# Performance work log

Hardware: AMD Instinct MI355X
Metric: run time of the kernel (lower is better)

## Reference

```python
import jax, jax.numpy as jnp
import numpy as np

B, T, D = 4, 2048, 1024
H = 16
HD = D // H  # 64
SCALE = 1.0 / np.sqrt(HD).astype(np.float32)


def setup_inputs() -> dict:
    key = jax.random.key(0)
    ks = jax.random.split(key, 5)
    std = 0.02
    return {
        "x": jax.random.normal(ks[0], (B, T, D), dtype=jnp.float32),
        "wq": jax.random.normal(ks[1], (D, D), dtype=jnp.float32) * std,
        "wk": jax.random.normal(ks[2], (D, D), dtype=jnp.float32) * std,
        "wv": jax.random.normal(ks[3], (D, D), dtype=jnp.float32) * std,
        "wo": jax.random.normal(ks[4], (D, D), dtype=jnp.float32) * std,
    }


def _shape(t):
    # [B,T,D] -> [B,H,T,HD]
    Bt, Tt, _ = t.shape
    return t.reshape(Bt, Tt, H, HD).transpose(0, 2, 1, 3)


def reference(x, wq, wk, wv, wo):
    # Linear layers are y = x @ W^T (torch nn.Linear semantics, no bias)
    q = _shape(x @ wq.T)  # [B,H,T,HD]
    k = _shape(x @ wk.T)
    v = _shape(x @ wv.T)
    att = jnp.einsum("bhqd,bhkd->bhqk", q, k) * SCALE  # [B,H,T,T]
    # causal mask: -inf strictly above diagonal
    causal = jnp.triu(jnp.full((T, T), -jnp.inf, dtype=att.dtype), k=1)
    att = att + causal[None, None, :, :]
    att = jax.nn.softmax(att.astype(jnp.float32), axis=-1).astype(att.dtype)
    # dropout prob = 0.0 -> identity
    y = jnp.einsum("bhqk,bhkd->bhqd", att, v)  # [B,H,T,HD]
    y = y.transpose(0, 2, 1, 3).reshape(B, T, D)
    return y @ wo.T
```

## Files before the change

kernel.cpp:

```cpp
#include <hip/hip_runtime.h>
#include <hip/hip_bf16.h>

#define BB 4
#define TT 2048
#define DDIM 1024
#define HH 16
#define HD 64

typedef __bf16 bf16_t;
typedef __bf16 bf16x4 __attribute__((ext_vector_type(4)));
typedef __bf16 bf16x8 __attribute__((ext_vector_type(8)));
typedef float f32x4 __attribute__((ext_vector_type(4)));

#define GLOAD_LDS(gp, lp) \
    __builtin_amdgcn_global_load_lds( \
        (const __attribute__((address_space(1))) void*)(gp), \
        (__attribute__((address_space(3))) void*)(lp), 16, 0, 0)

__global__ __launch_bounds__(256) void cvt_f32_bf16(
    const float* __restrict__ src, bf16_t* __restrict__ dst, size_t n8)
{
    size_t i = (size_t)blockIdx.x * blockDim.x + threadIdx.x;
    const size_t stride = (size_t)gridDim.x * blockDim.x;
    for (; i < n8; i += stride) {
        const f32x4 a = ((const f32x4*)src)[2 * i];
        const f32x4 b = ((const f32x4*)src)[2 * i + 1];
        bf16x8 v;
#pragma unroll
        for (int j = 0; j < 4; j++) { v[j] = (bf16_t)a[j]; v[4 + j] = (bf16_t)b[j]; }
        ((bf16x8*)dst)[i] = v;
    }
}

__global__ __launch_bounds__(256) void cvt_wpack(
    const float* __restrict__ s0, const float* __restrict__ s1,
    const float* __restrict__ s2, const float* __restrict__ s3,
    bf16_t* __restrict__ dst)
{
    const size_t n8 = (size_t)4 * DDIM * DDIM / 8;
    size_t i = (size_t)blockIdx.x * blockDim.x + threadIdx.x;
    const size_t stride = (size_t)gridDim.x * blockDim.x;
    for (; i < n8; i += stride) {
        const int sel = (int)(i >> 17);
        const float* s = sel == 0 ? s0 : sel == 1 ? s1 : sel == 2 ? s2 : s3;
        const size_t off8 = i & ((1u << 17) - 1);
        const f32x4 a = ((const f32x4*)s)[2 * off8];
        const f32x4 b = ((const f32x4*)s)[2 * off8 + 1];
        bf16x8 v;
#pragma unroll
        for (int j = 0; j < 4; j++) { v[j] = (bf16_t)a[j]; v[4 + j] = (bf16_t)b[j]; }
        ((bf16x8*)dst)[i] = v;
    }
}

__global__ __launch_bounds__(256) void gemm_qkv(
    const bf16_t* __restrict__ A, const bf16_t* __restrict__ Wqkv,
    bf16_t* __restrict__ Qo, bf16_t* __restrict__ Ko, bf16_t* __restrict__ Vto,
    int M, int K)
{
    __shared__ alignas(16) bf16_t As[128 * 32];
    __shared__ alignas(16) bf16_t Bs[128 * 32];

    const int tid  = threadIdx.x;
    const int lane = tid & 63;
    const int w    = tid >> 6;
    const int quad = lane >> 4;
    const int l15  = lane & 15;
    const int wm   = (w >> 1) * 64;
    const int wn   = (w & 1) * 64;
    const int tileN = blockIdx.x * 128;
    const int tileM = blockIdx.y * 128;

    const f32x4 vzero = {0.f, 0.f, 0.f, 0.f};
    f32x4 acc[4][4];
#pragma unroll
    for (int i = 0; i < 4; i++)
#pragma unroll
        for (int j = 0; j < 4; j++) acc[i][j] = vzero;

    const int lrow = lane >> 2;
    const int lcol = (lane & 3) * 8;

    for (int k0 = 0; k0 < K; k0 += 32) {
        __syncthreads();
#pragma unroll
        for (int q = 0; q < 2; q++) {
            const int r0 = w * 32 + q * 16;
            GLOAD_LDS(&A[(size_t)(tileM + r0 + lrow) * K + k0 + lcol], &As[r0 * 32]);
            GLOAD_LDS(&Wqkv[(size_t)(tileN + r0 + lrow) * K + k0 + lcol], &Bs[r0 * 32]);
        }
        __syncthreads();

        bf16x8 af[4], bf[4];
#pragma unroll
        for (int i = 0; i < 4; i++)
            af[i] = *(bf16x8*)&As[(wm + i * 16 + l15) * 32 + quad * 8];
#pragma unroll
        for (int j = 0; j < 4; j++)
            bf[j] = *(bf16x8*)&Bs[(wn + j * 16 + l15) * 32 + quad * 8];
#pragma unroll
        for (int i = 0; i < 4; i++)
#pragma unroll
            for (int j = 0; j < 4; j++)
                acc[i][j] = __builtin_amdgcn_mfma_f32_16x16x32_bf16(
                    af[i], bf[j], acc[i][j], 0, 0, 0);
    }

    const int region = tileN >> 10;
#pragma unroll
    for (int i = 0; i < 4; i++) {
        const int row = tileM + wm + i * 16 + quad * 4;
#pragma unroll
        for (int j = 0; j < 4; j++) {
            const int ncol = tileN + wn + j * 16 + l15;
            if (region == 2) {
                const int cl = ncol - 2048;
                const int h = cl >> 6, d = cl & 63;
                const int bb = row >> 11, tloc = row & (TT - 1);
                bf16x4 pk;
#pragma unroll
                for (int r = 0; r < 4; r++) pk[r] = (bf16_t)acc[i][j][r];
                *(bf16x4*)&Vto[(((size_t)bb * HH + h) * HD + d) * TT + tloc] = pk;
            } else {
                bf16_t* dst = (region == 0) ? Qo : Ko;
                const int cl = ncol & 1023;
#pragma unroll
                for (int r = 0; r < 4; r++)
                    dst[(size_t)(row + r) * DDIM + cl] = (bf16_t)acc[i][j][r];
            }
        }
    }
}

__global__ __launch_bounds__(256) void gemm_out(
    const bf16_t* __restrict__ A, const bf16_t* __restrict__ Bm,
    float* __restrict__ C, int M, int N, int K)
{
    __shared__ alignas(16) bf16_t As[64 * 32];
    __shared__ alignas(16) bf16_t Bs[128 * 32];

    const int tid  = threadIdx.x;
    const int lane = tid & 63;
    const int w    = tid >> 6;
    const int quad = lane >> 4;
    const int l15  = lane & 15;
    const int wm   = (w >> 1) * 32;
    const int wn   = (w & 1) * 64;
    const int tileN = blockIdx.x * 128;
    const int tileM = blockIdx.y * 64;

    const f32x4 vzero = {0.f, 0.f, 0.f, 0.f};
    f32x4 acc[2][4];
#pragma unroll
    for (int i = 0; i < 2; i++)
#pragma unroll
        for (int j = 0; j < 4; j++) acc[i][j] = vzero;

    const int lrow = lane >> 2;
    const int lcol = (lane & 3) * 8;

    for (int k0 = 0; k0 < K; k0 += 32) {
        __syncthreads();
        GLOAD_LDS(&A[(size_t)(tileM + w * 16 + lrow) * K + k0 + lcol], &As[w * 16 * 32]);
#pragma unroll
        for (int q = 0; q < 2; q++) {
            const int r0 = w * 32 + q * 16;
            GLOAD_LDS(&Bm[(size_t)(tileN + r0 + lrow) * K + k0 + lcol], &Bs[r0 * 32]);
        }
        __syncthreads();

        bf16x8 af[2], bf[4];
#pragma unroll
        for (int i = 0; i < 2; i++)
            af[i] = *(bf16x8*)&As[(wm + i * 16 + l15) * 32 + quad * 8];
#pragma unroll
        for (int j = 0; j < 4; j++)
            bf[j] = *(bf16x8*)&Bs[(wn + j * 16 + l15) * 32 + quad * 8];
#pragma unroll
        for (int i = 0; i < 2; i++)
#pragma unroll
            for (int j = 0; j < 4; j++)
                acc[i][j] = __builtin_amdgcn_mfma_f32_16x16x32_bf16(
                    af[i], bf[j], acc[i][j], 0, 0, 0);
    }

#pragma unroll
    for (int i = 0; i < 2; i++) {
#pragma unroll
        for (int r = 0; r < 4; r++) {
            const int row = tileM + wm + i * 16 + quad * 4 + r;
#pragma unroll
            for (int j = 0; j < 4; j++)
                C[(size_t)row * N + tileN + wn + j * 16 + l15] = acc[i][j][r];
        }
    }
}

__global__ __launch_bounds__(256, 4) void attn_causal(
    const bf16_t* __restrict__ Q, const bf16_t* __restrict__ Kg,
    const bf16_t* __restrict__ Vt_g, bf16_t* __restrict__ Y)
{
    __shared__ alignas(16) bf16_t Ks[64 * 72];
    __shared__ alignas(16) bf16_t Vt[64 * 72];
    __shared__ alignas(16) bf16_t Ps[4][16 * 72];

    const int tid  = threadIdx.x;
    const int lane = tid & 63;
    const int w    = tid >> 6;
    const int quad = lane >> 4;
    const int l15  = lane & 15;
    const int bh   = blockIdx.x;
    const int qp   = blockIdx.y;
    const int b = bh >> 4, h = bh & 15;

    const int stg_row = tid >> 3;
    const int stg_c8  = (tid & 7) * 8;

    const f32x4 vzero = {0.f, 0.f, 0.f, 0.f};
    bf16x8 ones;
#pragma unroll
    for (int j = 0; j < 8; j++) ones[j] = (l15 == 0) ? (bf16_t)1.0f : (bf16_t)0.0f;

#pragma unroll 1
    for (int half = 0; half < 2; half++) {
        const int qtile = half ? (31 - qp) : qp;
        const int qbase = qtile * 64;

        bf16x8 qf[2];
        {
            const size_t rq = (size_t)(b * TT + qbase + w * 16 + l15) * DDIM + h * 64;
            qf[0] = *(const bf16x8*)&Q[rq + quad * 8];
            qf[1] = *(const bf16x8*)&Q[rq + 32 + quad * 8];
        }

        f32x4 o[4], o4;
#pragma unroll
        for (int c = 0; c < 4; c++) o[c] = vzero;
        o4 = vzero;

        for (int kt = 0; kt <= qtile; kt++) {
            const int kbase = kt * 64;
            __syncthreads();
#pragma unroll
            for (int p = 0; p < 2; p++) {
                const int r = stg_row + p * 32;
                *(bf16x8*)&Ks[r * 72 + stg_c8] =
                    *(const bf16x8*)&Kg[(size_t)(b * TT + kbase + r) * DDIM + h * 64 + stg_c8];
                *(bf16x8*)&Vt[r * 72 + stg_c8] =
                    *(const bf16x8*)&Vt_g[((size_t)bh * HD + r) * TT + kbase + stg_c8];
            }
            __syncthreads();

            f32x4 s[4];
#pragma unroll
            for (int c = 0; c < 4; c++) {
                s[c] = vzero;
#pragma unroll
                for (int ss = 0; ss < 2; ss++) {
                    bf16x8 kf = *(bf16x8*)&Ks[(c * 16 + l15) * 72 + ss * 32 + quad * 8];
                    s[c] = __builtin_amdgcn_mfma_f32_16x16x32_bf16(qf[ss], kf, s[c], 0, 0, 0);
                }
            }

            const bool diag = (kt == qtile);
#pragma unroll
            for (int r = 0; r < 4; r++) {
                const int rrow = w * 16 + quad * 4 + r;
#pragma unroll
                for (int c = 0; c < 4; c++) {
                    float sv = s[c][r] * 0.125f;
                    if (diag && (c * 16 + l15 > rrow)) sv = -1e30f;
                    const int pchunk = (c * 2 + (l15 >> 3)) ^ quad;
                    Ps[w][(quad * 4 + r) * 72 + (pchunk << 3) + (l15 & 7)] =
                        (bf16_t)__expf(sv);
                }
            }

#pragma unroll
            for (int ss = 0; ss < 2; ss++) {
                bf16x8 pf = *(bf16x8*)&Ps[w][l15 * 72 +
                                             (((ss * 4 + quad) ^ (l15 >> 2)) << 3)];
#pragma unroll
                for (int c = 0; c < 4; c++) {
                    bf16x8 vf = *(bf16x8*)&Vt[(c * 16 + l15) * 72 + ss * 32 + quad * 8];
                    o[c] = __builtin_amdgcn_mfma_f32_16x16x32_bf16(pf, vf, o[c], 0, 0, 0);
                }
                o4 = __builtin_amdgcn_mfma_f32_16x16x32_bf16(pf, ones, o4, 0, 0, 0);
            }
        }

#pragma unroll
        for (int r = 0; r < 4; r++) {
            const float lsum = __shfl(o4[r], lane & 48, 64);
            const float inv = 1.0f / lsum;
            const int q = qbase + w * 16 + quad * 4 + r;
#pragma unroll
            for (int c = 0; c < 4; c++)
                Y[(size_t)(b * TT + q) * DDIM + h * 64 + c * 16 + l15] =
                    (bf16_t)(o[c][r] * inv);
        }
    }
}

extern "C" void kernel_launch(void* const* d_in, const int* in_sizes, int n_in,
                              void* d_out, int out_size, void* d_ws, size_t ws_size,
                              hipStream_t stream) {
    (void)in_sizes; (void)n_in; (void)out_size;
    const float* x  = (const float*)d_in[0];
    float* out = (float*)d_out;

    const int M = BB * TT;
    const size_t REGION = (size_t)M * DDIM;
    const size_t WREG   = (size_t)DDIM * DDIM;
    const size_t BATCH  = (size_t)TT * DDIM;
    bf16_t* ws = (bf16_t*)d_ws;

    if (ws_size >= (72ull << 20)) {
        bf16_t* xb  = ws;
        bf16_t* wpk = ws + REGION;
        bf16_t* Qb  = wpk + 4 * WREG;
        bf16_t* Kb  = Qb + REGION;
        bf16_t* Vtb = Kb + REGION;

        cvt_f32_bf16<<<1024, 256, 0, stream>>>(x, xb, REGION / 8);
        cvt_wpack<<<512, 256, 0, stream>>>(
            (const float*)d_in[1], (const float*)d_in[2],
            (const float*)d_in[3], (const float*)d_in[4], wpk);

        gemm_qkv<<<dim3(24, M / 128), 256, 0, stream>>>(
            xb, wpk, Qb, Kb, Vtb, M, DDIM);
        attn_causal<<<dim3(BB * HH, 16), 256, 0, stream>>>(Qb, Kb, Vtb, Qb);
        gemm_out<<<dim3(8, M / 64), 256, 0, stream>>>(
            Qb, wpk + 3 * WREG, out, M, DDIM, DDIM);
    } else {
        bf16_t* wpk = ws;
        bf16_t* xbb = ws + 4 * WREG;
        bf16_t* Qb  = xbb + BATCH;
        bf16_t* Kb  = Qb + BATCH;
        bf16_t* Vtb = Kb + BATCH;

        cvt_wpack<<<512, 256, 0, stream>>>(
            (const float*)d_in[1], (const float*)d_in[2],
            (const float*)d_in[3], (const float*)d_in[4], wpk);

        for (int b = 0; b < BB; b++) {
            const float* x_b = x + (size_t)b * BATCH;
            float* out_b = out + (size_t)b * BATCH;
            cvt_f32_bf16<<<512, 256, 0, stream>>>(x_b, xbb, BATCH / 8);
            gemm_qkv<<<dim3(24, TT / 128), 256, 0, stream>>>(
                xbb, wpk, Qb, Kb, Vtb, TT, DDIM);
            attn_causal<<<dim3(HH, 16), 256, 0, stream>>>(Qb, Kb, Vtb, Qb);
            gemm_out<<<dim3(8, TT / 64), 256, 0, stream>>>(
                Qb, wpk + 3 * WREG, out_b, TT, DDIM, DDIM);
        }
    }
}
```

Before: 272.1 us.

## Double GEMM K-tile with swizzled LDS and widen attention query strips to 128

Both projection GEMMs now stage 64-wide K slices per barrier pair instead of 32, using an XOR-swizzled LDS layout to avoid bank conflicts, which halves the number of sync points per tile. The attention kernel has each wave handle 32 query rows (two MFMA row blocks), so every K/V tile loaded into LDS is reused across twice as many queries, and the grid is halved to 8 strips per head. The cost is more registers and LDS per block; the occupancy hint drops from 4 to 2 blocks, and there are fewer attention blocks in flight.

After: 266.9 us. No clear change (-1.9%).

```diff
diff --git a/kernel.cpp b/kernel.cpp
--- a/kernel.cpp
+++ b/kernel.cpp
@@ -53,13 +53,21 @@
     }
 }
 
+__device__ __forceinline__ void stage8(const bf16_t* __restrict__ g, int ld,
+                                       bf16_t* __restrict__ ldsbase, int lane)
+{
+    const int rr = lane >> 3;
+    const int cc = (lane & 7) ^ ((rr & 1) << 2);
+    GLOAD_LDS(&g[(size_t)rr * ld + cc * 8], ldsbase);
+}
+
 __global__ __launch_bounds__(256) void gemm_qkv(
     const bf16_t* __restrict__ A, const bf16_t* __restrict__ Wqkv,
     bf16_t* __restrict__ Qo, bf16_t* __restrict__ Ko, bf16_t* __restrict__ Vto,
     int M, int K)
 {
-    __shared__ alignas(16) bf16_t As[128 * 32];
-    __shared__ alignas(16) bf16_t Bs[128 * 32];
+    __shared__ alignas(16) bf16_t As[128 * 64];
+    __shared__ alignas(16) bf16_t Bs[128 * 64];
 
     const int tid  = threadIdx.x;
     const int lane = tid & 63;
@@ -78,32 +86,35 @@
 #pragma unroll
         for (int j = 0; j < 4; j++) acc[i][j] = vzero;
 
-    const int lrow = lane >> 2;
-    const int lcol = (lane & 3) * 8;
-
-    for (int k0 = 0; k0 < K; k0 += 32) {
+    const int par4 = (l15 & 1) << 2;
+
+    for (int k0 = 0; k0 < K; k0 += 64) {
         __syncthreads();
 #pragma unroll
-        for (int q = 0; q < 2; q++) {
-            const int r0 = w * 32 + q * 16;
-            GLOAD_LDS(&A[(size_t)(tileM + r0 + lrow) * K + k0 + lcol], &As[r0 * 32]);
-            GLOAD_LDS(&Wqkv[(size_t)(tileN + r0 + lrow) * K + k0 + lcol], &Bs[r0 * 32]);
+        for (int q = 0; q < 4; q++) {
+            const int r0 = w * 32 + q * 8;
+            stage8(&A[(size_t)(tileM + r0) * K + k0], K, &As[r0 * 64], lane);
+            stage8(&Wqkv[(size_t)(tileN + r0) * K + k0], K, &Bs[r0 * 64], lane);
         }
         __syncthreads();
 
-        bf16x8 af[4], bf[4];
-#pragma unroll
-        for (int i = 0; i < 4; i++)
-            af[i] = *(bf16x8*)&As[(wm + i * 16 + l15) * 32 + quad * 8];
-#pragma unroll
-        for (int j = 0; j < 4; j++)
-            bf[j] = *(bf16x8*)&Bs[(wn + j * 16 + l15) * 32 + quad * 8];
-#pragma unroll
-        for (int i = 0; i < 4; i++)
+#pragma unroll
+        for (int ss = 0; ss < 2; ss++) {
+            const int phys = ((ss * 4 + quad) ^ par4) << 3;
+            bf16x8 af[4], bf[4];
+#pragma unroll
+            for (int i = 0; i < 4; i++)
+                af[i] = *(bf16x8*)&As[(wm + i * 16 + l15) * 64 + phys];
 #pragma unroll
             for (int j = 0; j < 4; j++)
-                acc[i][j] = __builtin_amdgcn_mfma_f32_16x16x32_bf16(
-                    af[i], bf[j], acc[i][j], 0, 0, 0);
+                bf[j] = *(bf16x8*)&Bs[(wn + j * 16 + l15) * 64 + phys];
+#pragma unroll
+            for (int i = 0; i < 4; i++)
+#pragma unroll
+                for (int j = 0; j < 4; j++)
+                    acc[i][j] = __builtin_amdgcn_mfma_f32_16x16x32_bf16(
+                        af[i], bf[j], acc[i][j], 0, 0, 0);
+        }
     }
 
     const int region = tileN >> 10;
@@ -136,8 +147,8 @@
     const bf16_t* __restrict__ A, const bf16_t* __restrict__ Bm,
     float* __restrict__ C, int M, int N, int K)
 {
-    __shared__ alignas(16) bf16_t As[64 * 32];
-    __shared__ alignas(16) bf16_t Bs[128 * 32];
+    __shared__ alignas(16) bf16_t As[64 * 64];
+    __shared__ alignas(16) bf16_t Bs[128 * 64];
 
     const int tid  = threadIdx.x;
     const int lane = tid & 63;
@@ -156,32 +167,39 @@
 #pragma unroll
         for (int j = 0; j < 4; j++) acc[i][j] = vzero;
 
-    const int lrow = lane >> 2;
-    const int lcol = (lane & 3) * 8;
-
-    for (int k0 = 0; k0 < K; k0 += 32) {
+    const int par4 = (l15 & 1) << 2;
+
+    for (int k0 = 0; k0 < K; k0 += 64) {
         __syncthreads();
-        GLOAD_LDS(&A[(size_t)(tileM + w * 16 + lrow) * K + k0 + lcol], &As[w * 16 * 32]);
 #pragma unroll
         for (int q = 0; q < 2; q++) {
-            const int r0 = w * 32 + q * 16;
-            GLOAD_LDS(&Bm[(size_t)(tileN + r0 + lrow) * K + k0 + lcol], &Bs[r0 * 32]);
+            const int r0 = w * 16 + q * 8;
+            stage8(&A[(size_t)(tileM + r0) * K + k0], K, &As[r0 * 64], lane);
+        }
+#pragma unroll
+        for (int q = 0; q < 4; q++) {
+            const int r0 = w * 32 + q * 8;
+            stage8(&Bm[(size_t)(tileN + r0) * K + k0], K, &Bs[r0 * 64], lane);
         }
         __syncthreads();
 
-        bf16x8 af[2], bf[4];
-#pragma unroll
-        for (int i = 0; i < 2; i++)
-            af[i] = *(bf16x8*)&As[(wm + i * 16 + l15) * 32 + quad * 8];
-#pragma unroll
-        for (int j = 0; j < 4; j++)
-            bf[j] = *(bf16x8*)&Bs[(wn + j * 16 + l15) * 32 + quad * 8];
-#pragma unroll
-        for (int i = 0; i < 2; i++)
+#pragma unroll
+        for (int ss = 0; ss < 2; ss++) {
+            const int phys = ((ss * 4 + quad) ^ par4) << 3;
+            bf16x8 af[2], bf[4];
+#pragma unroll
+            for (int i = 0; i < 2; i++)
+                af[i] = *(bf16x8*)&As[(wm + i * 16 + l15) * 64 + phys];
 #pragma unroll
             for (int j = 0; j < 4; j++)
-                acc[i][j] = __builtin_amdgcn_mfma_f32_16x16x32_bf16(
-                    af[i], bf[j], acc[i][j], 0, 0, 0);
+                bf[j] = *(bf16x8*)&Bs[(wn + j * 16 + l15) * 64 + phys];
+#pragma unroll
+            for (int i = 0; i < 2; i++)
+#pragma unroll
+                for (int j = 0; j < 4; j++)
+                    acc[i][j] = __builtin_amdgcn_mfma_f32_16x16x32_bf16(
+                        af[i], bf[j], acc[i][j], 0, 0, 0);
+        }
     }
 
 #pragma unroll
@@ -196,13 +214,13 @@
     }
 }
 
-__global__ __launch_bounds__(256, 4) void attn_causal(
+__global__ __launch_bounds__(256, 2) void attn_causal(
     const bf16_t* __restrict__ Q, const bf16_t* __restrict__ Kg,
     const bf16_t* __restrict__ Vt_g, bf16_t* __restrict__ Y)
 {
     __shared__ alignas(16) bf16_t Ks[64 * 72];
     __shared__ alignas(16) bf16_t Vt[64 * 72];
-    __shared__ alignas(16) bf16_t Ps[4][16 * 72];
+    __shared__ alignas(16) bf16_t Ps[4][32 * 72];
 
     const int tid  = threadIdx.x;
     const int lane = tid & 63;
@@ -210,7 +228,7 @@
     const int quad = lane >> 4;
     const int l15  = lane & 15;
     const int bh   = blockIdx.x;
-    const int qp   = blockIdx.y;
+    const int sp   = blockIdx.y;
     const int b = bh >> 4, h = bh & 15;
 
     const int stg_row = tid >> 3;
@@ -223,22 +241,28 @@
 
 #pragma unroll 1
     for (int half = 0; half < 2; half++) {
-        const int qtile = half ? (31 - qp) : qp;
-        const int qbase = qtile * 64;
-
-        bf16x8 qf[2];
-        {
-            const size_t rq = (size_t)(b * TT + qbase + w * 16 + l15) * DDIM + h * 64;
-            qf[0] = *(const bf16x8*)&Q[rq + quad * 8];
-            qf[1] = *(const bf16x8*)&Q[rq + 32 + quad * 8];
-        }
-
-        f32x4 o[4], o4;
-#pragma unroll
-        for (int c = 0; c < 4; c++) o[c] = vzero;
-        o4 = vzero;
-
-        for (int kt = 0; kt <= qtile; kt++) {
+        const int strip = half ? (15 - sp) : sp;
+        const int qbase = strip * 128;
+
+        bf16x8 qf[2][2];
+#pragma unroll
+        for (int mi = 0; mi < 2; mi++) {
+            const size_t rq =
+                (size_t)(b * TT + qbase + w * 32 + mi * 16 + l15) * DDIM + h * 64;
+            qf[mi][0] = *(const bf16x8*)&Q[rq + quad * 8];
+            qf[mi][1] = *(const bf16x8*)&Q[rq + 32 + quad * 8];
+        }
+
+        f32x4 o[2][4], o4[2];
+#pragma unroll
+        for (int mi = 0; mi < 2; mi++) {
+#pragma unroll
+            for (int c = 0; c < 4; c++) o[mi][c] = vzero;
+            o4[mi] = vzero;
+        }
+
+        const int nkt = 2 * strip + 2;
+        for (int kt = 0; kt < nkt; kt++) {
             const int kbase = kt * 64;
             __syncthreads();
 #pragma unroll
@@ -251,53 +275,75 @@
             }
             __syncthreads();
 
-            f32x4 s[4];
+            f32x4 s[2][4];
 #pragma unroll
             for (int c = 0; c < 4; c++) {
-                s[c] = vzero;
-#pragma unroll
-                for (int ss = 0; ss < 2; ss++) {
-                    bf16x8 kf = *(bf16x8*)&Ks[(c * 16 + l15) * 72 + ss * 32 + quad * 8];
-                    s[c] = __builtin_amdgcn_mfma_f32_16x16x32_bf16(qf[ss], kf, s[c], 0, 0, 0);
+                bf16x8 kf0 = *(bf16x8*)&Ks[(c * 16 + l15) * 72 + quad * 8];
+                bf16x8 kf1 = *(bf16x8*)&Ks[(c * 16 + l15) * 72 + 32 + quad * 8];
+#pragma unroll
+                for (int mi = 0; mi < 2; mi++) {
+                    f32x4 t = __builtin_amdgcn_mfma_f32_16x16x32_bf16(
+                        qf[mi][0], kf0, vzero, 0, 0, 0);
+                    s[mi][c] = __builtin_amdgcn_mfma_f32_16x16x32_bf16(
+                        qf[mi][1], kf1, t, 0, 0, 0);
                 }
             }
 
-            const bool diag = (kt == qtile);
-#pragma unroll
-            for (int r = 0; r < 4; r++) {
-                const int rrow = w * 16 + quad * 4 + r;
-#pragma unroll
-                for (int c = 0; c < 4; c++) {
-                    float sv = s[c][r] * 0.125f;
-                    if (diag && (c * 16 + l15 > rrow)) sv = -1e30f;
-                    const int pchunk = (c * 2 + (l15 >> 3)) ^ quad;
-                    Ps[w][(quad * 4 + r) * 72 + (pchunk << 3) + (l15 & 7)] =
-                        (bf16_t)__expf(sv);
+#pragma unroll
+            for (int mi = 0; mi < 2; mi++) {
+                const int qlow = qbase + w * 32 + mi * 16;
+                const bool need = (kbase + 63 > qlow);
+#pragma unroll
+                for (int r = 0; r < 4; r++) {
+                    const int qrow = qlow + quad * 4 + r;
+                    const int prow = mi * 16 + quad * 4 + r;
+#pragma unroll
+                    for (int c = 0; c < 4; c++) {
+                        float sv = s[mi][c][r] * 0.125f;
+                        if (need && (kbase + c * 16 + l15 > qrow)) sv = -1e30f;
+                        const int pchunk = (c * 2 + (l15 >> 3)) ^ (prow >> 2);
+                        Ps[w][prow * 72 + (pchunk << 3) + (l15 & 7)] =
+                            (bf16_t)__expf(sv);
+                    }
                 }
             }
 
 #pragma unroll
             for (int ss = 0; ss < 2; ss++) {
-                bf16x8 pf = *(bf16x8*)&Ps[w][l15 * 72 +
-                                             (((ss * 4 + quad) ^ (l15 >> 2)) << 3)];
+                bf16x8 pf[2];
+#pragma unroll
+                for (int mi = 0; mi < 2; mi++) {
+                    const int m = mi * 16 + l15;
+                    pf[mi] = *(bf16x8*)&Ps[w][m * 72 +
+                                              ((((ss * 4 + quad) ^ (m >> 2)) & 7) << 3)];
+                }
 #pragma unroll
                 for (int c = 0; c < 4; c++) {
                     bf16x8 vf = *(bf16x8*)&Vt[(c * 16 + l15) * 72 + ss * 32 + quad * 8];
-                    o[c] = __builtin_amdgcn_mfma_f32_16x16x32_bf16(pf, vf, o[c], 0, 0, 0);
+#pragma unroll
+                    for (int mi = 0; mi < 2; mi++)
+                        o[mi][c] = __builtin_amdgcn_mfma_f32_16x16x32_bf16(
+                            pf[mi], vf, o[mi][c], 0, 0, 0);
                 }
-                o4 = __builtin_amdgcn_mfma_f32_16x16x32_bf16(pf, ones, o4, 0, 0, 0);
-            }
-        }
-
-#pragma unroll
-        for (int r = 0; r < 4; r++) {
-            const float lsum = __shfl(o4[r], lane & 48, 64);
-            const float inv = 1.0f / lsum;
-            const int q = qbase + w * 16 + quad * 4 + r;
-#pragma unroll
-            for (int c = 0; c < 4; c++)
-                Y[(size_t)(b * TT + q) * DDIM + h * 64 + c * 16 + l15] =
-                    (bf16_t)(o[c][r] * inv);
+#pragma unroll
+                for (int mi = 0; mi < 2; mi++)
+                    o4[mi] = __builtin_amdgcn_mfma_f32_16x16x32_bf16(
+                        pf[mi], ones, o4[mi], 0, 0, 0);
+            }
+        }
+
+#pragma unroll
+        for (int mi = 0; mi < 2; mi++) {
+#pragma unroll
+            for (int r = 0; r < 4; r++) {
+                const float lsum = __shfl(o4[mi][r], lane & 48, 64);
+                const float inv = 1.0f / lsum;
+                const int q = qbase + w * 32 + mi * 16 + quad * 4 + r;
+#pragma unroll
+                for (int c = 0; c < 4; c++)
+                    Y[(size_t)(b * TT + q) * DDIM + h * 64 + c * 16 + l15] =
+                        (bf16_t)(o[mi][c][r] * inv);
+            }
         }
     }
 }
@@ -329,7 +375,7 @@
 
         gemm_qkv<<<dim3(24, M / 128), 256, 0, stream>>>(
             xb, wpk, Qb, Kb, Vtb, M, DDIM);
-        attn_causal<<<dim3(BB * HH, 16), 256, 0, stream>>>(Qb, Kb, Vtb, Qb);
+        attn_causal<<<dim3(BB * HH, 8), 256, 0, stream>>>(Qb, Kb, Vtb, Qb);
         gemm_out<<<dim3(8, M / 64), 256, 0, stream>>>(
             Qb, wpk + 3 * WREG, out, M, DDIM, DDIM);
     } else {
@@ -349,7 +395,7 @@
             cvt_f32_bf16<<<512, 256, 0, stream>>>(x_b, xbb, BATCH / 8);
             gemm_qkv<<<dim3(24, TT / 128), 256, 0, stream>>>(
                 xbb, wpk, Qb, Kb, Vtb, TT, DDIM);
-            attn_causal<<<dim3(HH, 16), 256, 0, stream>>>(Qb, Kb, Vtb, Qb);
+            attn_causal<<<dim3(HH, 8), 256, 0, stream>>>(Qb, Kb, Vtb, Qb);
             gemm_out<<<dim3(8, TT / 64), 256, 0, stream>>>(
                 Qb, wpk + 3 * WREG, out_b, TT, DDIM, DDIM);
         }
```
